# Kernel optimization log

Measured on AMD Instinct MI355X. Metric: run time of the kernel, lower is better.

Reference implementation:

```python
import jax, jax.numpy as jnp
import numpy as np

B, N, ND, ED, TD, H = 4, 256, 256, 64, 64, 8
D = ND // H
SCALE = np.float32(1.0 / np.sqrt(ND))
EPS = 1e-5


def leaky(x):
    return jnp.where(x >= 0, x, 0.05 * x)


def _ln(x, g, b):
    m = x.mean(axis=-1, keepdims=True)
    v = ((x - m) ** 2).mean(axis=-1, keepdims=True)
    return (x - m) * jax.lax.rsqrt(v + EPS) * g + b


def setup_inputs() -> dict:
    key = jax.random.key(0)
    ks = iter(jax.random.split(key, 64))

    def w(shape):
        return (jax.random.normal(next(ks), shape, jnp.float32) * 0.02).astype(jnp.float32)

    inp = {
        'nodes': jax.random.normal(next(ks), (B, N, ND), jnp.float32),
        'edges': jax.random.normal(next(ks), (B, N, N, ED), jnp.float32),
        'times': jax.random.normal(next(ks), (B, TD), jnp.float32),
        'Wq': w((ND + TD, ND)), 'bq': w((ND,)),
        'Wk': w((ND + TD, ND)), 'bk': w((ND,)),
        'Wv': w((ND + TD, ND)), 'bv': w((ND,)),
        'Wm': w((ED, ND)), 'bm': w((ND,)),
        'Wa': w((ED, ND)), 'ba': w((ND,)),
        'Wno': w((ND, ND)), 'bno': w((ND,)),
        'Weo': w((ND, ED)), 'beo': w((ED,)),
        'ln1n_g': jnp.ones((ND,), jnp.float32), 'ln1n_b': jnp.zeros((ND,), jnp.float32),
        'ln1e_g': jnp.ones((ED,), jnp.float32), 'ln1e_b': jnp.zeros((ED,), jnp.float32),
        'Wn1': w((ND, ND)), 'bn1': w((ND,)),
        'Wn2': w((ND, ND)), 'bn2': w((ND,)),
        'We1': w((ED, ED)), 'be1': w((ED,)),
        'We2': w((ED, ED)), 'be2': w((ED,)),
        'ln2n_g': jnp.ones((ND,), jnp.float32), 'ln2n_b': jnp.zeros((ND,), jnp.float32),
        'ln2e_g': jnp.ones((ED,), jnp.float32), 'ln2e_b': jnp.zeros((ED,), jnp.float32),
    }
    return inp


def reference(nodes, edges, times, Wq, bq, Wk, bk, Wv, bv, Wm, bm, Wa, ba,
              Wno, bno, Weo, beo, ln1n_g, ln1n_b, ln1e_g, ln1e_b,
              Wn1, bn1, Wn2, bn2, We1, be1, We2, be2,
              ln2n_g, ln2n_b, ln2e_g, ln2e_b):
    b, n, _ = nodes.shape
    # concat time embedding onto every node: [B, N, ND+TD]
    nt = jnp.concatenate([nodes, jnp.broadcast_to(times[:, None, :], (b, n, times.shape[-1]))], axis=-1)
    q = (nt @ Wq + bq).reshape(b, n, H, D)
    k = (nt @ Wk + bk).reshape(b, n, H, D)
    # all-pairs elementwise qk product: [B, N, N, H, D]
    attn = q[:, :, None, :, :] * k[:, None, :, :, :] * SCALE
    em = (edges @ Wm + bm).reshape(b, n, n, H, D)
    ea = (edges @ Wa + ba).reshape(b, n, n, H, D)
    new_edges = attn * em + attn + ea                    # [B,N,N,H,D]
    a = jax.nn.softmax(new_edges.sum(axis=4), axis=2)    # [B,N,N,H]
    v = (nt @ Wv + bv).reshape(b, n, H, D)
    wv = jnp.einsum('bijh,bjhd->bihd', a, v).reshape(b, n, ND)
    ne_flat = new_edges.reshape(b, n, n, ND)
    attn_nodes = wv @ Wno + bno                          # lin_nodes_out
    attn_edges = leaky(ne_flat) @ Weo + beo              # lin_edges_out
    attn_nodes = leaky(_ln(attn_nodes + nodes, ln1n_g, ln1n_b))
    attn_edges = _ln(attn_edges + edges, ln1e_g, ln1e_b)
    mn = leaky(attn_nodes @ Wn1 + bn1) @ Wn2 + bn2
    me = leaky(attn_edges @ We1 + be1) @ We2 + be2
    out_nodes = leaky(_ln(mn + attn_nodes, ln2n_g, ln2n_b))
    out_edges = _ln(me + attn_edges, ln2e_g, ln2e_b)
    return out_nodes, out_edges
```

## Files before the change

kernel.cpp:

```cpp
#include <hip/hip_runtime.h>
#include <hip/hip_bf16.h>

#define DEVFN __device__ __forceinline__

static constexpr float KSCALE = 0.0625f;
static constexpr float KEPS   = 1e-5f;

static constexpr int WS_Q   = 0;
static constexpr int WS_K   = 262144;
static constexpr int WS_V   = 524288;
static constexpr int WS_WNO = 1048576;
static constexpr int WS_WN1 = WS_WNO + 65536;
static constexpr int WS_WN2 = WS_WN1 + 65536;
static constexpr int WS_P   = WS_WN2 + 65536;
static constexpr int P_BQ=0, P_BK=256, P_BV=512, P_BM=768, P_BA=1024, P_BNO=1280,
  P_BEO=1536, P_LN1NG=1600, P_LN1NB=1856, P_LN1EG=2112, P_LN1EB=2176,
  P_BN1=2240, P_BN2=2496, P_BE1=2752, P_BE2=2816, P_LN2NG=2880, P_LN2NB=3136,
  P_LN2EG=3392, P_LN2EB=3456;
static constexpr int WS_BF  = WS_P + 3520;

typedef __attribute__((ext_vector_type(8))) short short8v;
typedef __attribute__((ext_vector_type(4))) float f32x4;
typedef __attribute__((ext_vector_type(4))) unsigned uint4v;
#define MFMA16(a, b, c) __builtin_amdgcn_mfma_f32_16x16x32_bf16((a), (b), (c), 0, 0, 0)

DEVFN float ldin(const void* p, int i, int bf) {
  if (bf) {
    unsigned short u = ((const unsigned short*)p)[i];
    return __uint_as_float(((unsigned)u) << 16);
  }
  return ((const float*)p)[i];
}
DEVFN unsigned short f2bf(float x) {
  unsigned b = __float_as_uint(x);
  b += 0x7FFFu + ((b >> 16) & 1u);
  return (unsigned short)(b >> 16);
}
DEVFN float bf2f(unsigned short u) { return __uint_as_float(((unsigned)u) << 16); }
DEVFN float lrelu(float x) { return x >= 0.f ? x : 0.05f * x; }
DEVFN int   dtflag(const void* l1ng) {
  return (((const unsigned*)l1ng)[0] != 0x3F800000u) ? 1 : 0;
}
DEVFN unsigned pack_bf2(float a, float b) {
  return ((unsigned)f2bf(b) << 16) | (unsigned)f2bf(a);
}
DEVFN short8v pack8(const float* p) {
  const float4 x0 = *(const float4*)p;
  const float4 x1 = *(const float4*)(p + 4);
  uint4v d;
  d[0] = pack_bf2(x0.x, x0.y); d[1] = pack_bf2(x0.z, x0.w);
  d[2] = pack_bf2(x1.x, x1.y); d[3] = pack_bf2(x1.z, x1.w);
  return __builtin_bit_cast(short8v, d);
}

__global__ __launch_bounds__(256) void k0_prep(float* __restrict__ wsf,
    const void* Wq, const void* bq, const void* Wk, const void* bk,
    const void* Wv, const void* bv, const void* Wm, const void* bm,
    const void* Wa, const void* ba, const void* Wno, const void* bno,
    const void* Weo, const void* beo, const void* l1ng, const void* l1nb,
    const void* l1eg, const void* l1eb, const void* Wn1, const void* bn1,
    const void* Wn2, const void* bn2, const void* We1, const void* be1,
    const void* We2, const void* be2, const void* l2ng, const void* l2nb,
    const void* l2eg, const void* l2eb)
{
  const int bf = dtflag(l1ng);
  const int g  = blockIdx.x * blockDim.x + threadIdx.x;
  const int gs = gridDim.x * blockDim.x;
  short* sb = (short*)(wsf + WS_BF);
#define CPY(src, off, n) for (int i = g; i < (n); i += gs) wsf[(off) + i] = ldin(src, i, bf)
  for (int i = g; i < 16384; i += gs) {
    int c = i >> 6, t = i & 63;
    sb[i]         = (short)f2bf(ldin(Wm, t * 256 + c, bf));
    sb[16384 + i] = (short)f2bf(ldin(Wa, t * 256 + c, bf));
  }
  for (int i = g; i < 16384; i += gs) {
    int u = i >> 8, c = i & 255;
    sb[32768 + i] = (short)f2bf(ldin(Weo, c * 64 + u, bf));
  }
  for (int i = g; i < 4096; i += gs) {
    int u = i >> 6, t = i & 63;
    sb[49152 + i] = (short)f2bf(ldin(We1, t * 64 + u, bf));
    sb[53248 + i] = (short)f2bf(ldin(We2, t * 64 + u, bf));
  }
  for (int i = g; i < 81920; i += gs) {
    int c = i / 320, t = i - c * 320;
    const int src = t * 256 + c;
    sb[57344 + i]  = (short)f2bf(ldin(Wq, src, bf));
    sb[139264 + i] = (short)f2bf(ldin(Wk, src, bf));
    sb[221184 + i] = (short)f2bf(ldin(Wv, src, bf));
  }
  CPY(Wno, WS_WNO, 65536);
  CPY(Wn1, WS_WN1, 65536);
  CPY(Wn2, WS_WN2, 65536);
  CPY(bq,  WS_P + P_BQ, 256);   CPY(bk,  WS_P + P_BK, 256);
  CPY(bv,  WS_P + P_BV, 256);   CPY(bm,  WS_P + P_BM, 256);
  CPY(ba,  WS_P + P_BA, 256);   CPY(bno, WS_P + P_BNO, 256);
  CPY(beo, WS_P + P_BEO, 64);
  CPY(l1ng, WS_P + P_LN1NG, 256); CPY(l1nb, WS_P + P_LN1NB, 256);
  CPY(l1eg, WS_P + P_LN1EG, 64);  CPY(l1eb, WS_P + P_LN1EB, 64);
  CPY(bn1, WS_P + P_BN1, 256);  CPY(bn2, WS_P + P_BN2, 256);
  CPY(be1, WS_P + P_BE1, 64);   CPY(be2, WS_P + P_BE2, 64);
  CPY(l2ng, WS_P + P_LN2NG, 256); CPY(l2nb, WS_P + P_LN2NB, 256);
  CPY(l2eg, WS_P + P_LN2EG, 64);  CPY(l2eb, WS_P + P_LN2EB, 64);
#undef CPY
}

__global__ __launch_bounds__(256) void k1_qkv(float* __restrict__ wsf,
    const void* nodes, const void* times, const void* l1ng)
{
  const int bf  = dtflag(l1ng);
  const int bid = blockIdx.x;
  const int b   = bid / 48;
  const int rem = bid - b * 48;
  const int mat = rem >> 4;
  const int n16 = rem & 15;
  const int tid = threadIdx.x;
  const int wv_ = tid >> 6;
  const int l   = tid & 63;
  const int l15 = l & 15, gq = l >> 4;

  const float* Pb = wsf + WS_P;
  const short* At = (const short*)(wsf + WS_BF) + 57344 + mat * 81920;
  const int n = (n16 << 4) + l15;

  short8v Bn[10];
  if (bf) {
    const unsigned short* np = (const unsigned short*)nodes + (size_t)(b * 256 + n) * 256;
#pragma unroll
    for (int kb = 0; kb < 8; ++kb)
      Bn[kb] = *(const short8v*)(np + (kb << 5) + (gq << 3));
    const unsigned short* tp = (const unsigned short*)times + b * 64;
#pragma unroll
    for (int kb = 8; kb < 10; ++kb)
      Bn[kb] = *(const short8v*)(tp + ((kb - 8) << 5) + (gq << 3));
  } else {
    const float* np = (const float*)nodes + (size_t)(b * 256 + n) * 256;
#pragma unroll
    for (int kb = 0; kb < 8; ++kb)
      Bn[kb] = pack8(np + (kb << 5) + (gq << 3));
    const float* tp = (const float*)times + b * 64;
#pragma unroll
    for (int kb = 8; kb < 10; ++kb)
      Bn[kb] = pack8(tp + ((kb - 8) << 5) + (gq << 3));
  }

  f32x4 acc[4];
#pragma unroll
  for (int cf = 0; cf < 4; ++cf) acc[cf] = f32x4{0.f, 0.f, 0.f, 0.f};
#pragma unroll
  for (int cf = 0; cf < 4; ++cf) {
    const int crow = ((wv_ << 6) + (cf << 4) + l15) * 320;
#pragma unroll
    for (int kb = 0; kb < 10; ++kb) {
      const short8v A = *(const short8v*)(At + crow + (kb << 5) + (gq << 3));
      acc[cf] = MFMA16(A, Bn[kb], acc[cf]);
    }
  }

  if (mat == 1) {
    float* dst = wsf + WS_K + b * 65536;
#pragma unroll
    for (int cf = 0; cf < 4; ++cf)
#pragma unroll
      for (int r = 0; r < 4; ++r) {
        const int c = (wv_ << 6) + (cf << 4) + (gq << 2) + r;
        dst[c * 256 + n] = acc[cf][r] + Pb[P_BK + c];
      }
  } else if (mat == 0) {
    float* dst = wsf + WS_Q + (size_t)(b * 256 + n) * 256;
#pragma unroll
    for (int cf = 0; cf < 4; ++cf)
#pragma unroll
      for (int r = 0; r < 4; ++r) {
        const int c = (wv_ << 6) + (cf << 4) + (gq << 2) + r;
        dst[c] = (acc[cf][r] + Pb[P_BQ + c]) * KSCALE;
      }
  } else {
    float* dst = wsf + WS_V + (size_t)(b * 256 + n) * 256;
#pragma unroll
    for (int cf = 0; cf < 4; ++cf)
#pragma unroll
      for (int r = 0; r < 4; ++r) {
        const int c = (wv_ << 6) + (cf << 4) + (gq << 2) + r;
        dst[c] = acc[cf][r] + Pb[P_BV + c];
      }
  }
}

DEVFN void bstats256(float v, float* red, float& mu, float& rs) {
  float s = v, q = v * v;
#pragma unroll
  for (int off = 32; off; off >>= 1) { s += __shfl_xor(s, off, 64); q += __shfl_xor(q, off, 64); }
  const int w = threadIdx.x >> 6;
  if ((threadIdx.x & 63) == 0) { red[w] = s; red[8 + w] = q; }
  __syncthreads();
  s = red[0] + red[1] + red[2] + red[3];
  q = red[8] + red[9] + red[10] + red[11];
  __syncthreads();
  mu = s * (1.f / 256.f);
  const float var = q * (1.f / 256.f) - mu * mu;
  rs = rsqrtf(var + KEPS);
}

__global__ __launch_bounds__(256, 2) void k2_edges(float* __restrict__ wsf,
    const void* edges, const void* nodes, void* __restrict__ out, const void* l1ng)
{
  const int bf  = dtflag(l1ng);
  const int bid = blockIdx.x;
  const int b   = bid >> 8;
  const int tid = threadIdx.x;
  const int wv_ = tid >> 6;
  const int l   = tid & 63;
  const int l15 = l & 15, gq = l >> 4;

  __shared__ float sl[8 * 256];
  __shared__ unsigned short ptile[4][4096];
  __shared__ float swv[256];
  __shared__ float red[16];

  const float* Pb = wsf + WS_P;
  const short* WmTb  = (const short*)(wsf + WS_BF);
  const short* WaTb  = WmTb + 16384;
  const short* WeoTb = WaTb + 16384;
  const short* We1Tb = WeoTb + 16384;
  const short* We2Tb = We1Tb + 4096;
  const float* kTb   = wsf + WS_K + b * 65536;

#pragma unroll
  for (int h = 0; h < 8; ++h) sl[(h << 8) + tid] = 0.f;

  short8v Ef[2][4];
#pragma unroll
  for (int jf = 0; jf < 4; ++jf) {
    const int jg = (wv_ << 6) + (jf << 4) + l15;
    const size_t ebase = (size_t)(bid * 256 + jg) * 64;
#pragma unroll
    for (int kb = 0; kb < 2; ++kb) {
      const int t0 = (kb << 5) + (gq << 3);
      if (bf) {
        Ef[kb][jf] = *(const short8v*)((const unsigned short*)edges + ebase + t0);
      } else {
        Ef[kb][jf] = pack8((const float*)edges + ebase + t0);
      }
    }
  }

  f32x4 Oacc[4][4];
#pragma unroll
  for (int uf = 0; uf < 4; ++uf)
#pragma unroll
    for (int jf = 0; jf < 4; ++jf) { Oacc[uf][jf] = f32x4{0.f, 0.f, 0.f, 0.f}; }

  char* myp = (char*)&ptile[wv_][0];
  const int swz = (l15 & 7) << 4;

#pragma unroll 1
  for (int chunk = 0; chunk < 4; ++chunk) {
#pragma unroll
    for (int ci = 0; ci < 4; ++ci) {
      const int cf = (chunk << 2) + ci;
      const int crow = ((cf << 4) + l15) << 6;
      const short8v Am0 = *(const short8v*)(WmTb + crow + (gq << 3));
      const short8v Am1 = *(const short8v*)(WmTb + crow + 32 + (gq << 3));
      const short8v Aa0 = *(const short8v*)(WaTb + crow + (gq << 3));
      const short8v Aa1 = *(const short8v*)(WaTb + crow + 32 + (gq << 3));
      const int ce = (cf << 4) + (gq << 2);
      const float4 q4  = *(const float4*)(wsf + WS_Q + (size_t)bid * 256 + ce);
      const float4 bm4 = *(const float4*)(Pb + P_BM + ce);
      const float4 ba4 = *(const float4*)(Pb + P_BA + ce);
      const int h = cf >> 1;
#pragma unroll
      for (int jf = 0; jf < 4; ++jf) {
        f32x4 em = f32x4{0.f, 0.f, 0.f, 0.f};
        f32x4 ea = f32x4{0.f, 0.f, 0.f, 0.f};
        em = MFMA16(Am0, Ef[0][jf], em);
        em = MFMA16(Am1, Ef[1][jf], em);
        ea = MFMA16(Aa0, Ef[0][jf], ea);
        ea = MFMA16(Aa1, Ef[1][jf], ea);
        const int jg = (wv_ << 6) + (jf << 4) + l15;
        const float kv0 = kTb[(ce + 0) * 256 + jg];
        const float kv1 = kTb[(ce + 1) * 256 + jg];
        const float kv2 = kTb[(ce + 2) * 256 + jg];
        const float kv3 = kTb[(ce + 3) * 256 + jg];
        const float ne0 = (q4.x * kv0) * (em[0] + bm4.x + 1.f) + (ea[0] + ba4.x);
        const float ne1 = (q4.y * kv1) * (em[1] + bm4.y + 1.f) + (ea[1] + ba4.y);
        const float ne2 = (q4.z * kv2) * (em[2] + bm4.z + 1.f) + (ea[2] + ba4.z);
        const float ne3 = (q4.w * kv3) * (em[3] + bm4.w + 1.f) + (ea[3] + ba4.w);
        float part = (ne0 + ne1) + (ne2 + ne3);
        part += __shfl_xor(part, 16, 64);
        part += __shfl_xor(part, 32, 64);
        if (gq == 0) sl[(h << 8) + jg] += part;
        const unsigned pd0 = pack_bf2(lrelu(ne0), lrelu(ne1));
        const unsigned pd1 = pack_bf2(lrelu(ne2), lrelu(ne3));
        const int jl = (jf << 4) + l15;
        const unsigned boff = (jl << 7) + ((unsigned)((ci << 5) + (gq << 3)) ^ swz);
        *(unsigned long long*)(myp + boff) = ((unsigned long long)pd1 << 32) | pd0;
      }
    }
    short8v Bp[2][4];
#pragma unroll
    for (int kb = 0; kb < 2; ++kb)
#pragma unroll
      for (int jf = 0; jf < 4; ++jf) {
        const int jl = (jf << 4) + l15;
        const unsigned boff = (jl << 7) + ((unsigned)((kb << 6) + (gq << 4)) ^ swz);
        Bp[kb][jf] = *(const short8v*)(myp + boff);
      }
#pragma unroll
    for (int uf = 0; uf < 4; ++uf) {
      const int urow = ((uf << 4) + l15) << 8;
      const int cb = chunk << 6;
      const short8v Aw0 = *(const short8v*)(WeoTb + urow + cb + (gq << 3));
      const short8v Aw1 = *(const short8v*)(WeoTb + urow + cb + 32 + (gq << 3));
#pragma unroll
      for (int jf = 0; jf < 4; ++jf) {
        Oacc[uf][jf] = MFMA16(Aw0, Bp[0][jf], Oacc[uf][jf]);
        Oacc[uf][jf] = MFMA16(Aw1, Bp[1][jf], Oacc[uf][jf]);
      }
    }
  }

#pragma unroll
  for (int uf = 0; uf < 4; ++uf)
#pragma unroll
    for (int jf = 0; jf < 4; ++jf) {
      const unsigned pd0 = pack_bf2(Oacc[uf][jf][0], Oacc[uf][jf][1]);
      const unsigned pd1 = pack_bf2(Oacc[uf][jf][2], Oacc[uf][jf][3]);
      const int jl = (jf << 4) + l15;
      const unsigned boff = (jl << 7) + ((unsigned)((uf << 5) + (gq << 3)) ^ swz);
      *(unsigned long long*)(myp + boff) = ((unsigned long long)pd1 << 32) | pd0;
    }

  __syncthreads();

  {
    const int h = tid >> 5, ll = tid & 31;
    float* row = sl + (h << 8);
    float pv[8];
    float m = -1e30f;
#pragma unroll
    for (int k2 = 0; k2 < 8; ++k2) { float x = row[ll + (k2 << 5)]; pv[k2] = x; m = fmaxf(m, x); }
#pragma unroll
    for (int off = 16; off; off >>= 1) m = fmaxf(m, __shfl_xor(m, off, 64));
    float sum = 0.f;
#pragma unroll
    for (int k2 = 0; k2 < 8; ++k2) { float p = __expf(pv[k2] - m); pv[k2] = p; sum += p; }
#pragma unroll
    for (int off = 16; off; off >>= 1) sum += __shfl_xor(sum, off, 64);
    const float inv = 1.f / sum;
#pragma unroll
    for (int k2 = 0; k2 < 8; ++k2) row[ll + (k2 << 5)] = pv[k2] * inv;
  }
  __syncthreads();

  {
    const int c = tid;
    const float* arow = sl + ((c >> 5) << 8);
    const float* vcol = wsf + WS_V + b * 65536 + c;
    float a0 = 0.f, a1 = 0.f, a2 = 0.f, a3 = 0.f;
    for (int jj = 0; jj < 256; jj += 4) {
      a0 = fmaf(arow[jj],     vcol[jj << 8],        a0);
      a1 = fmaf(arow[jj + 1], vcol[(jj + 1) << 8],  a1);
      a2 = fmaf(arow[jj + 2], vcol[(jj + 2) << 8],  a2);
      a3 = fmaf(arow[jj + 3], vcol[(jj + 3) << 8],  a3);
    }
    swv[c] = (a0 + a1) + (a2 + a3);
  }

  const int jl   = tid & 63;
  const int rswz = (jl & 7) << 4;
  float e[64];
  {
    float o[64];
#pragma unroll
    for (int s = 0; s < 8; ++s) {
      const short8v v = *(const short8v*)(myp + (jl << 7) + ((unsigned)(s << 4) ^ rswz));
#pragma unroll
      for (int e2 = 0; e2 < 8; ++e2) o[(s << 3) + e2] = bf2f((unsigned short)v[e2]);
    }
    const size_t ebase = (size_t)(bid * 256 + tid) * 64;
    if (bf) {
      const unsigned short* ep = (const unsigned short*)edges + ebase;
#pragma unroll
      for (int t = 0; t < 64; ++t) e[t] = bf2f(ep[t]);
    } else {
      const float4* ep = (const float4*)((const float*)edges + ebase);
#pragma unroll
      for (int t = 0; t < 16; ++t) {
        const float4 v4 = ep[t];
        e[4*t] = v4.x; e[4*t+1] = v4.y; e[4*t+2] = v4.z; e[4*t+3] = v4.w;
      }
    }
#pragma unroll
    for (int u = 0; u < 64; ++u) o[u] = o[u] + Pb[P_BEO + u] + e[u];
    float mu = 0.f;
#pragma unroll
    for (int u = 0; u < 64; ++u) mu += o[u];
    mu *= (1.f / 64.f);
    float s2 = 0.f;
#pragma unroll
    for (int u = 0; u < 64; ++u) { float d = o[u] - mu; s2 = fmaf(d, d, s2); }
    const float rs = rsqrtf(s2 * (1.f / 64.f) + KEPS);
#pragma unroll
    for (int u = 0; u < 64; ++u) e[u] = fmaf((o[u] - mu) * rs, Pb[P_LN1EG + u], Pb[P_LN1EB + u]);
#pragma unroll
    for (int u0 = 0; u0 < 64; u0 += 4) {
      const unsigned pd0 = pack_bf2(e[u0],     e[u0 + 1]);
      const unsigned pd1 = pack_bf2(e[u0 + 2], e[u0 + 3]);
      *(unsigned long long*)(myp + (jl << 7) + ((unsigned)(u0 << 1) ^ rswz)) =
        ((unsigned long long)pd1 << 32) | pd0;
    }
  }

  {
    short8v Bf[2][4];
#pragma unroll
    for (int kb = 0; kb < 2; ++kb)
#pragma unroll
      for (int jf = 0; jf < 4; ++jf) {
        const int jfl = (jf << 4) + l15;
        Bf[kb][jf] = *(const short8v*)(myp + (jfl << 7) + ((unsigned)((kb << 6) + (gq << 4)) ^ swz));
      }
    f32x4 Hc[4][4];
#pragma unroll
    for (int uf = 0; uf < 4; ++uf) {
      const int ur = ((uf << 4) + l15) << 6;
      const short8v A0 = *(const short8v*)(We1Tb + ur + (gq << 3));
      const short8v A1 = *(const short8v*)(We1Tb + ur + 32 + (gq << 3));
#pragma unroll
      for (int jf = 0; jf < 4; ++jf) {
        f32x4 hh = f32x4{0.f, 0.f, 0.f, 0.f};
        hh = MFMA16(A0, Bf[0][jf], hh);
        hh = MFMA16(A1, Bf[1][jf], hh);
        Hc[uf][jf] = hh;
      }
    }
#pragma unroll
    for (int uf = 0; uf < 4; ++uf) {
      const int u0 = (uf << 4) + (gq << 2);
      const float4 b14 = *(const float4*)(Pb + P_BE1 + u0);
#pragma unroll
      for (int jf = 0; jf < 4; ++jf) {
        const int jfl = (jf << 4) + l15;
        const unsigned pd0 = pack_bf2(lrelu(Hc[uf][jf][0] + b14.x), lrelu(Hc[uf][jf][1] + b14.y));
        const unsigned pd1 = pack_bf2(lrelu(Hc[uf][jf][2] + b14.z), lrelu(Hc[uf][jf][3] + b14.w));
        *(unsigned long long*)(myp + (jfl << 7) + ((unsigned)((uf << 5) + (gq << 3)) ^ swz)) =
          ((unsigned long long)pd1 << 32) | pd0;
      }
    }
#pragma unroll
    for (int kb = 0; kb < 2; ++kb)
#pragma unroll
      for (int jf = 0; jf < 4; ++jf) {
        const int jfl = (jf << 4) + l15;
        Bf[kb][jf] = *(const short8v*)(myp + (jfl << 7) + ((unsigned)((kb << 6) + (gq << 4)) ^ swz));
      }
#pragma unroll
    for (int uf = 0; uf < 4; ++uf) {
      const int ur = ((uf << 4) + l15) << 6;
      const short8v A0 = *(const short8v*)(We2Tb + ur + (gq << 3));
      const short8v A1 = *(const short8v*)(We2Tb + ur + 32 + (gq << 3));
      const int u0 = (uf << 4) + (gq << 2);
      const float4 b24 = *(const float4*)(Pb + P_BE2 + u0);
#pragma unroll
      for (int jf = 0; jf < 4; ++jf) {
        f32x4 mm = f32x4{0.f, 0.f, 0.f, 0.f};
        mm = MFMA16(A0, Bf[0][jf], mm);
        mm = MFMA16(A1, Bf[1][jf], mm);
        const int jfl = (jf << 4) + l15;
        const unsigned pd0 = pack_bf2(mm[0] + b24.x, mm[1] + b24.y);
        const unsigned pd1 = pack_bf2(mm[2] + b24.z, mm[3] + b24.w);
        *(unsigned long long*)(myp + (jfl << 7) + ((unsigned)((uf << 5) + (gq << 3)) ^ swz)) =
          ((unsigned long long)pd1 << 32) | pd0;
      }
    }
  }

  {
    float o[64];
#pragma unroll
    for (int s = 0; s < 8; ++s) {
      const short8v v = *(const short8v*)(myp + (jl << 7) + ((unsigned)(s << 4) ^ rswz));
#pragma unroll
      for (int e2 = 0; e2 < 8; ++e2) o[(s << 3) + e2] = bf2f((unsigned short)v[e2]);
    }
#pragma unroll
    for (int u = 0; u < 64; ++u) o[u] += e[u];
    float mu = 0.f;
#pragma unroll
    for (int u = 0; u < 64; ++u) mu += o[u];
    mu *= (1.f / 64.f);
    float s2 = 0.f;
#pragma unroll
    for (int u = 0; u < 64; ++u) { float d = o[u] - mu; s2 = fmaf(d, d, s2); }
    const float rs = rsqrtf(s2 * (1.f / 64.f) + KEPS);
    if (bf) {
      unsigned* op = (unsigned*)((unsigned short*)out + 262144 + (size_t)(bid * 256 + tid) * 64);
#pragma unroll
      for (int u = 0; u < 64; u += 2) {
        const float y0 = fmaf((o[u]     - mu) * rs, Pb[P_LN2EG + u],     Pb[P_LN2EB + u]);
        const float y1 = fmaf((o[u + 1] - mu) * rs, Pb[P_LN2EG + u + 1], Pb[P_LN2EB + u + 1]);
        op[u >> 1] = ((unsigned)f2bf(y1) << 16) | (unsigned)f2bf(y0);
      }
    } else {
      float4* op = (float4*)((float*)out + 262144 + (size_t)(bid * 256 + tid) * 64);
#pragma unroll
      for (int u = 0; u < 64; u += 4) {
        float4 y;
        y.x = fmaf((o[u]     - mu) * rs, Pb[P_LN2EG + u],     Pb[P_LN2EB + u]);
        y.y = fmaf((o[u + 1] - mu) * rs, Pb[P_LN2EG + u + 1], Pb[P_LN2EB + u + 1]);
        y.z = fmaf((o[u + 2] - mu) * rs, Pb[P_LN2EG + u + 2], Pb[P_LN2EB + u + 2]);
        y.w = fmaf((o[u + 3] - mu) * rs, Pb[P_LN2EG + u + 3], Pb[P_LN2EB + u + 3]);
        op[u >> 2] = y;
      }
    }
  }

  __syncthreads();
  {
    const int c = tid;
    float an = Pb[P_BNO + c];
    {
      const float* w = wsf + WS_WNO + c;
      float p0 = 0.f, p1 = 0.f, p2 = 0.f, p3 = 0.f;
      for (int t = 0; t < 256; t += 4) {
        p0 = fmaf(swv[t],     w[t << 8],       p0);
        p1 = fmaf(swv[t + 1], w[(t + 1) << 8], p1);
        p2 = fmaf(swv[t + 2], w[(t + 2) << 8], p2);
        p3 = fmaf(swv[t + 3], w[(t + 3) << 8], p3);
      }
      an += (p0 + p1) + (p2 + p3);
    }
    an += ldin(nodes, bid * 256 + c, bf);
    float mu, rs;
    bstats256(an, red, mu, rs);
    const float anf = lrelu(fmaf((an - mu) * rs, Pb[P_LN1NG + c], Pb[P_LN1NB + c]));
    __syncthreads();
    swv[c] = anf;
    __syncthreads();
    float h1 = Pb[P_BN1 + c];
    {
      const float* w = wsf + WS_WN1 + c;
      float p0 = 0.f, p1 = 0.f, p2 = 0.f, p3 = 0.f;
      for (int t = 0; t < 256; t += 4) {
        p0 = fmaf(swv[t],     w[t << 8],       p0);
        p1 = fmaf(swv[t + 1], w[(t + 1) << 8], p1);
        p2 = fmaf(swv[t + 2], w[(t + 2) << 8], p2);
        p3 = fmaf(swv[t + 3], w[(t + 3) << 8], p3);
      }
      h1 += (p0 + p1) + (p2 + p3);
    }
    h1 = lrelu(h1);
    __syncthreads();
    swv[c] = h1;
    __syncthreads();
    float mn = Pb[P_BN2 + c];
    {
      const float* w = wsf + WS_WN2 + c;
      float p0 = 0.f, p1 = 0.f, p2 = 0.f, p3 = 0.f;
      for (int t = 0; t < 256; t += 4) {
        p0 = fmaf(swv[t],     w[t << 8],       p0);
        p1 = fmaf(swv[t + 1], w[(t + 1) << 8], p1);
        p2 = fmaf(swv[t + 2], w[(t + 2) << 8], p2);
        p3 = fmaf(swv[t + 3], w[(t + 3) << 8], p3);
      }
      mn += (p0 + p1) + (p2 + p3);
    }
    const float x2 = mn + anf;
    bstats256(x2, red, mu, rs);
    const float y = lrelu(fmaf((x2 - mu) * rs, Pb[P_LN2NG + c], Pb[P_LN2NB + c]));
    if (bf) ((unsigned short*)out)[bid * 256 + c] = f2bf(y);
    else    ((float*)out)[bid * 256 + c] = y;
  }
}

extern "C" void kernel_launch(void* const* d_in, const int* in_sizes, int n_in,
                              void* d_out, int out_size, void* d_ws, size_t ws_size,
                              hipStream_t stream) {
  (void)in_sizes; (void)n_in; (void)out_size; (void)ws_size;
  float* wsf = (float*)d_ws;
  const void* nodes = d_in[0];
  const void* edges = d_in[1];
  const void* times = d_in[2];
  const void* l1ng  = d_in[17];

  k0_prep<<<128, 256, 0, stream>>>(wsf,
      d_in[3],  d_in[4],  d_in[5],  d_in[6],  d_in[7],  d_in[8],
      d_in[9],  d_in[10], d_in[11], d_in[12], d_in[13], d_in[14],
      d_in[15], d_in[16], d_in[17], d_in[18], d_in[19], d_in[20],
      d_in[21], d_in[22], d_in[23], d_in[24], d_in[25], d_in[26],
      d_in[27], d_in[28], d_in[29], d_in[30], d_in[31], d_in[32]);
  k1_qkv<<<192, 256, 0, stream>>>(wsf, nodes, times, l1ng);
  k2_edges<<<1024, 256, 0, stream>>>(wsf, edges, nodes, d_out, l1ng);
}
```

Measured before the change: 191.2 us.

## Double k2_edges block to 512 threads, splitting j rows and row-LN across lanes

The edge kernel now runs 512 threads per block, so each wave handles 32 edge rows instead of 64. Per-row LayerNorm work is split across two half-waves with a shuffle reduction, and the node-side matvecs and attention-weighted V sum are split in halves and combined through shared memory. The aim is to cut per-thread register pressure (the large float[64] arrays) and raise latency hiding. The cost is extra __syncthreads and partial-sum reductions, and launch_bounds(512,4) may force register spills.

```diff
diff --git a/kernel.cpp b/kernel.cpp
--- a/kernel.cpp
+++ b/kernel.cpp
@@ -187,22 +187,22 @@
   }
 }
 
-DEVFN void bstats256(float v, float* red, float& mu, float& rs) {
-  float s = v, q = v * v;
-#pragma unroll
-  for (int off = 32; off; off >>= 1) { s += __shfl_xor(s, off, 64); q += __shfl_xor(q, off, 64); }
-  const int w = threadIdx.x >> 6;
-  if ((threadIdx.x & 63) == 0) { red[w] = s; red[8 + w] = q; }
+DEVFN void bstats256_512(float v, float* red, int tid, float& mu, float& rs) {
+  if (tid < 256) {
+    float s = v, q = v * v;
+#pragma unroll
+    for (int off = 32; off; off >>= 1) { s += __shfl_xor(s, off, 64); q += __shfl_xor(q, off, 64); }
+    if ((tid & 63) == 0) { red[tid >> 6] = s; red[8 + (tid >> 6)] = q; }
+  }
   __syncthreads();
-  s = red[0] + red[1] + red[2] + red[3];
-  q = red[8] + red[9] + red[10] + red[11];
+  const float ss = (red[0] + red[1]) + (red[2] + red[3]);
+  const float qq = (red[8] + red[9]) + (red[10] + red[11]);
   __syncthreads();
-  mu = s * (1.f / 256.f);
-  const float var = q * (1.f / 256.f) - mu * mu;
-  rs = rsqrtf(var + KEPS);
-}
-
-__global__ __launch_bounds__(256, 2) void k2_edges(float* __restrict__ wsf,
+  mu = ss * (1.f / 256.f);
+  rs = rsqrtf(qq * (1.f / 256.f) - mu * mu + KEPS);
+}
+
+__global__ __launch_bounds__(512, 4) void k2_edges(float* __restrict__ wsf,
     const void* edges, const void* nodes, void* __restrict__ out, const void* l1ng)
 {
   const int bf  = dtflag(l1ng);
@@ -214,8 +214,9 @@
   const int l15 = l & 15, gq = l >> 4;
 
   __shared__ float sl[8 * 256];
-  __shared__ unsigned short ptile[4][4096];
+  __shared__ unsigned short ptile[8][2048];
   __shared__ float swv[256];
+  __shared__ float swv2[512];
   __shared__ float red[16];
 
   const float* Pb = wsf + WS_P;
@@ -227,12 +228,13 @@
   const float* kTb   = wsf + WS_K + b * 65536;
 
 #pragma unroll
-  for (int h = 0; h < 8; ++h) sl[(h << 8) + tid] = 0.f;
-
-  short8v Ef[2][4];
-#pragma unroll
-  for (int jf = 0; jf < 4; ++jf) {
-    const int jg = (wv_ << 6) + (jf << 4) + l15;
+  for (int i = 0; i < 4; ++i) sl[tid + (i << 9)] = 0.f;
+  __syncthreads();
+
+  short8v Ef[2][2];
+#pragma unroll
+  for (int jf = 0; jf < 2; ++jf) {
+    const int jg = (wv_ << 5) + (jf << 4) + l15;
     const size_t ebase = (size_t)(bid * 256 + jg) * 64;
 #pragma unroll
     for (int kb = 0; kb < 2; ++kb) {
@@ -245,11 +247,11 @@
     }
   }
 
-  f32x4 Oacc[4][4];
+  f32x4 Oacc[4][2];
 #pragma unroll
   for (int uf = 0; uf < 4; ++uf)
 #pragma unroll
-    for (int jf = 0; jf < 4; ++jf) { Oacc[uf][jf] = f32x4{0.f, 0.f, 0.f, 0.f}; }
+    for (int jf = 0; jf < 2; ++jf) { Oacc[uf][jf] = f32x4{0.f, 0.f, 0.f, 0.f}; }
 
   char* myp = (char*)&ptile[wv_][0];
   const int swz = (l15 & 7) << 4;
@@ -270,14 +272,14 @@
       const float4 ba4 = *(const float4*)(Pb + P_BA + ce);
       const int h = cf >> 1;
 #pragma unroll
-      for (int jf = 0; jf < 4; ++jf) {
+      for (int jf = 0; jf < 2; ++jf) {
         f32x4 em = f32x4{0.f, 0.f, 0.f, 0.f};
         f32x4 ea = f32x4{0.f, 0.f, 0.f, 0.f};
         em = MFMA16(Am0, Ef[0][jf], em);
         em = MFMA16(Am1, Ef[1][jf], em);
         ea = MFMA16(Aa0, Ef[0][jf], ea);
         ea = MFMA16(Aa1, Ef[1][jf], ea);
-        const int jg = (wv_ << 6) + (jf << 4) + l15;
+        const int jg = (wv_ << 5) + (jf << 4) + l15;
         const float kv0 = kTb[(ce + 0) * 256 + jg];
         const float kv1 = kTb[(ce + 1) * 256 + jg];
         const float kv2 = kTb[(ce + 2) * 256 + jg];
@@ -297,11 +299,11 @@
         *(unsigned long long*)(myp + boff) = ((unsigned long long)pd1 << 32) | pd0;
       }
     }
-    short8v Bp[2][4];
+    short8v Bp[2][2];
 #pragma unroll
     for (int kb = 0; kb < 2; ++kb)
 #pragma unroll
-      for (int jf = 0; jf < 4; ++jf) {
+      for (int jf = 0; jf < 2; ++jf) {
         const int jl = (jf << 4) + l15;
         const unsigned boff = (jl << 7) + ((unsigned)((kb << 6) + (gq << 4)) ^ swz);
         Bp[kb][jf] = *(const short8v*)(myp + boff);
@@ -313,7 +315,7 @@
       const short8v Aw0 = *(const short8v*)(WeoTb + urow + cb + (gq << 3));
       const short8v Aw1 = *(const short8v*)(WeoTb + urow + cb + 32 + (gq << 3));
 #pragma unroll
-      for (int jf = 0; jf < 4; ++jf) {
+      for (int jf = 0; jf < 2; ++jf) {
         Oacc[uf][jf] = MFMA16(Aw0, Bp[0][jf], Oacc[uf][jf]);
         Oacc[uf][jf] = MFMA16(Aw1, Bp[1][jf], Oacc[uf][jf]);
       }
@@ -323,7 +325,7 @@
 #pragma unroll
   for (int uf = 0; uf < 4; ++uf)
 #pragma unroll
-    for (int jf = 0; jf < 4; ++jf) {
+    for (int jf = 0; jf < 2; ++jf) {
       const unsigned pd0 = pack_bf2(Oacc[uf][jf][0], Oacc[uf][jf][1]);
       const unsigned pd1 = pack_bf2(Oacc[uf][jf][2], Oacc[uf][jf][3]);
       const int jl = (jf << 4) + l15;
@@ -334,101 +336,112 @@
   __syncthreads();
 
   {
-    const int h = tid >> 5, ll = tid & 31;
+    const int h = wv_;
     float* row = sl + (h << 8);
-    float pv[8];
+    float pv[4];
     float m = -1e30f;
 #pragma unroll
-    for (int k2 = 0; k2 < 8; ++k2) { float x = row[ll + (k2 << 5)]; pv[k2] = x; m = fmaxf(m, x); }
-#pragma unroll
-    for (int off = 16; off; off >>= 1) m = fmaxf(m, __shfl_xor(m, off, 64));
+    for (int k2 = 0; k2 < 4; ++k2) { float x = row[l + (k2 << 6)]; pv[k2] = x; m = fmaxf(m, x); }
+#pragma unroll
+    for (int off = 32; off; off >>= 1) m = fmaxf(m, __shfl_xor(m, off, 64));
     float sum = 0.f;
 #pragma unroll
-    for (int k2 = 0; k2 < 8; ++k2) { float p = __expf(pv[k2] - m); pv[k2] = p; sum += p; }
-#pragma unroll
-    for (int off = 16; off; off >>= 1) sum += __shfl_xor(sum, off, 64);
+    for (int k2 = 0; k2 < 4; ++k2) { float p = __expf(pv[k2] - m); pv[k2] = p; sum += p; }
+#pragma unroll
+    for (int off = 32; off; off >>= 1) sum += __shfl_xor(sum, off, 64);
     const float inv = 1.f / sum;
 #pragma unroll
-    for (int k2 = 0; k2 < 8; ++k2) row[ll + (k2 << 5)] = pv[k2] * inv;
+    for (int k2 = 0; k2 < 4; ++k2) row[l + (k2 << 6)] = pv[k2] * inv;
   }
   __syncthreads();
 
   {
-    const int c = tid;
+    const int c = tid & 255, jh = tid >> 8;
     const float* arow = sl + ((c >> 5) << 8);
     const float* vcol = wsf + WS_V + b * 65536 + c;
+    const int j0 = jh << 7;
     float a0 = 0.f, a1 = 0.f, a2 = 0.f, a3 = 0.f;
-    for (int jj = 0; jj < 256; jj += 4) {
+    for (int jj = j0; jj < j0 + 128; jj += 4) {
       a0 = fmaf(arow[jj],     vcol[jj << 8],        a0);
       a1 = fmaf(arow[jj + 1], vcol[(jj + 1) << 8],  a1);
       a2 = fmaf(arow[jj + 2], vcol[(jj + 2) << 8],  a2);
       a3 = fmaf(arow[jj + 3], vcol[(jj + 3) << 8],  a3);
     }
-    swv[c] = (a0 + a1) + (a2 + a3);
-  }
-
-  const int jl   = tid & 63;
-  const int rswz = (jl & 7) << 4;
-  float e[64];
+    swv2[tid] = (a0 + a1) + (a2 + a3);
+  }
+  __syncthreads();
+  if (tid < 256) swv[tid] = swv2[tid] + swv2[tid + 256];
+
+  const int r    = l & 31;
+  const int hf   = l >> 5;
+  const int jrow = (wv_ << 5) + r;
+  const int u0   = hf << 5;
+  const int rswz = (r & 7) << 4;
+  float ae[32];
   {
-    float o[64];
-#pragma unroll
-    for (int s = 0; s < 8; ++s) {
-      const short8v v = *(const short8v*)(myp + (jl << 7) + ((unsigned)(s << 4) ^ rswz));
-#pragma unroll
-      for (int e2 = 0; e2 < 8; ++e2) o[(s << 3) + e2] = bf2f((unsigned short)v[e2]);
-    }
-    const size_t ebase = (size_t)(bid * 256 + tid) * 64;
+    float xr[32];
+#pragma unroll
+    for (int s4 = 0; s4 < 4; ++s4) {
+      const int s = (hf << 2) + s4;
+      const short8v v = *(const short8v*)(myp + (r << 7) + ((unsigned)(s << 4) ^ rswz));
+#pragma unroll
+      for (int e2 = 0; e2 < 8; ++e2) xr[(s4 << 3) + e2] = bf2f((unsigned short)v[e2]);
+    }
+    const size_t ebase = (size_t)(bid * 256 + jrow) * 64 + u0;
     if (bf) {
       const unsigned short* ep = (const unsigned short*)edges + ebase;
 #pragma unroll
-      for (int t = 0; t < 64; ++t) e[t] = bf2f(ep[t]);
+      for (int k = 0; k < 32; ++k) xr[k] += Pb[P_BEO + u0 + k] + bf2f(ep[k]);
     } else {
-      const float4* ep = (const float4*)((const float*)edges + ebase);
-#pragma unroll
-      for (int t = 0; t < 16; ++t) {
-        const float4 v4 = ep[t];
-        e[4*t] = v4.x; e[4*t+1] = v4.y; e[4*t+2] = v4.z; e[4*t+3] = v4.w;
-      }
-    }
-#pragma unroll
-    for (int u = 0; u < 64; ++u) o[u] = o[u] + Pb[P_BEO + u] + e[u];
-    float mu = 0.f;
-#pragma unroll
-    for (int u = 0; u < 64; ++u) mu += o[u];
-    mu *= (1.f / 64.f);
-    float s2 = 0.f;
-#pragma unroll
-    for (int u = 0; u < 64; ++u) { float d = o[u] - mu; s2 = fmaf(d, d, s2); }
-    const float rs = rsqrtf(s2 * (1.f / 64.f) + KEPS);
-#pragma unroll
-    for (int u = 0; u < 64; ++u) e[u] = fmaf((o[u] - mu) * rs, Pb[P_LN1EG + u], Pb[P_LN1EB + u]);
-#pragma unroll
-    for (int u0 = 0; u0 < 64; u0 += 4) {
-      const unsigned pd0 = pack_bf2(e[u0],     e[u0 + 1]);
-      const unsigned pd1 = pack_bf2(e[u0 + 2], e[u0 + 3]);
-      *(unsigned long long*)(myp + (jl << 7) + ((unsigned)(u0 << 1) ^ rswz)) =
+      const float* ep = (const float*)edges + ebase;
+#pragma unroll
+      for (int k = 0; k < 32; k += 4) {
+        const float4 v4 = *(const float4*)(ep + k);
+        xr[k]     += Pb[P_BEO + u0 + k]     + v4.x;
+        xr[k + 1] += Pb[P_BEO + u0 + k + 1] + v4.y;
+        xr[k + 2] += Pb[P_BEO + u0 + k + 2] + v4.z;
+        xr[k + 3] += Pb[P_BEO + u0 + k + 3] + v4.w;
+      }
+    }
+    float s = 0.f;
+#pragma unroll
+    for (int k = 0; k < 32; ++k) s += xr[k];
+    s += __shfl_xor(s, 32, 64);
+    const float mu = s * (1.f / 64.f);
+    float q = 0.f;
+#pragma unroll
+    for (int k = 0; k < 32; ++k) { const float d = xr[k] - mu; q = fmaf(d, d, q); }
+    q += __shfl_xor(q, 32, 64);
+    const float rstd = rsqrtf(q * (1.f / 64.f) + KEPS);
+#pragma unroll
+    for (int k = 0; k < 32; ++k)
+      ae[k] = fmaf((xr[k] - mu) * rstd, Pb[P_LN1EG + u0 + k], Pb[P_LN1EB + u0 + k]);
+#pragma unroll
+    for (int k = 0; k < 32; k += 4) {
+      const unsigned pd0 = pack_bf2(ae[k],     ae[k + 1]);
+      const unsigned pd1 = pack_bf2(ae[k + 2], ae[k + 3]);
+      *(unsigned long long*)(myp + (r << 7) + ((unsigned)((u0 + k) << 1) ^ rswz)) =
         ((unsigned long long)pd1 << 32) | pd0;
     }
   }
 
   {
-    short8v Bf[2][4];
+    short8v Bf[2][2];
 #pragma unroll
     for (int kb = 0; kb < 2; ++kb)
 #pragma unroll
-      for (int jf = 0; jf < 4; ++jf) {
+      for (int jf = 0; jf < 2; ++jf) {
         const int jfl = (jf << 4) + l15;
         Bf[kb][jf] = *(const short8v*)(myp + (jfl << 7) + ((unsigned)((kb << 6) + (gq << 4)) ^ swz));
       }
-    f32x4 Hc[4][4];
+    f32x4 Hc[4][2];
 #pragma unroll
     for (int uf = 0; uf < 4; ++uf) {
       const int ur = ((uf << 4) + l15) << 6;
       const short8v A0 = *(const short8v*)(We1Tb + ur + (gq << 3));
       const short8v A1 = *(const short8v*)(We1Tb + ur + 32 + (gq << 3));
 #pragma unroll
-      for (int jf = 0; jf < 4; ++jf) {
+      for (int jf = 0; jf < 2; ++jf) {
         f32x4 hh = f32x4{0.f, 0.f, 0.f, 0.f};
         hh = MFMA16(A0, Bf[0][jf], hh);
         hh = MFMA16(A1, Bf[1][jf], hh);
@@ -437,10 +450,10 @@
     }
 #pragma unroll
     for (int uf = 0; uf < 4; ++uf) {
-      const int u0 = (uf << 4) + (gq << 2);
-      const float4 b14 = *(const float4*)(Pb + P_BE1 + u0);
-#pragma unroll
-      for (int jf = 0; jf < 4; ++jf) {
+      const int uu = (uf << 4) + (gq << 2);
+      const float4 b14 = *(const float4*)(Pb + P_BE1 + uu);
+#pragma unroll
+      for (int jf = 0; jf < 2; ++jf) {
         const int jfl = (jf << 4) + l15;
         const unsigned pd0 = pack_bf2(lrelu(Hc[uf][jf][0] + b14.x), lrelu(Hc[uf][jf][1] + b14.y));
         const unsigned pd1 = pack_bf2(lrelu(Hc[uf][jf][2] + b14.z), lrelu(Hc[uf][jf][3] + b14.w));
@@ -451,7 +464,7 @@
 #pragma unroll
     for (int kb = 0; kb < 2; ++kb)
 #pragma unroll
-      for (int jf = 0; jf < 4; ++jf) {
+      for (int jf = 0; jf < 2; ++jf) {
         const int jfl = (jf << 4) + l15;
         Bf[kb][jf] = *(const short8v*)(myp + (jfl << 7) + ((unsigned)((kb << 6) + (gq << 4)) ^ swz));
       }
@@ -460,10 +473,10 @@
       const int ur = ((uf << 4) + l15) << 6;
       const short8v A0 = *(const short8v*)(We2Tb + ur + (gq << 3));
       const short8v A1 = *(const short8v*)(We2Tb + ur + 32 + (gq << 3));
-      const int u0 = (uf << 4) + (gq << 2);
-      const float4 b24 = *(const float4*)(Pb + P_BE2 + u0);
-#pragma unroll
-      for (int jf = 0; jf < 4; ++jf) {
+      const int uu = (uf << 4) + (gq << 2);
+      const float4 b24 = *(const float4*)(Pb + P_BE2 + uu);
+#pragma unroll
+      for (int jf = 0; jf < 2; ++jf) {
         f32x4 mm = f32x4{0.f, 0.f, 0.f, 0.f};
         mm = MFMA16(A0, Bf[0][jf], mm);
         mm = MFMA16(A1, Bf[1][jf], mm);
@@ -477,100 +490,109 @@
   }
 
   {
-    float o[64];
-#pragma unroll
-    for (int s = 0; s < 8; ++s) {
-      const short8v v = *(const short8v*)(myp + (jl << 7) + ((unsigned)(s << 4) ^ rswz));
-#pragma unroll
-      for (int e2 = 0; e2 < 8; ++e2) o[(s << 3) + e2] = bf2f((unsigned short)v[e2]);
-    }
-#pragma unroll
-    for (int u = 0; u < 64; ++u) o[u] += e[u];
-    float mu = 0.f;
-#pragma unroll
-    for (int u = 0; u < 64; ++u) mu += o[u];
-    mu *= (1.f / 64.f);
-    float s2 = 0.f;
-#pragma unroll
-    for (int u = 0; u < 64; ++u) { float d = o[u] - mu; s2 = fmaf(d, d, s2); }
-    const float rs = rsqrtf(s2 * (1.f / 64.f) + KEPS);
+    float xr[32];
+#pragma unroll
+    for (int s4 = 0; s4 < 4; ++s4) {
+      const int s = (hf << 2) + s4;
+      const short8v v = *(const short8v*)(myp + (r << 7) + ((unsigned)(s << 4) ^ rswz));
+#pragma unroll
+      for (int e2 = 0; e2 < 8; ++e2) xr[(s4 << 3) + e2] = bf2f((unsigned short)v[e2]);
+    }
+#pragma unroll
+    for (int k = 0; k < 32; ++k) xr[k] += ae[k];
+    float s = 0.f;
+#pragma unroll
+    for (int k = 0; k < 32; ++k) s += xr[k];
+    s += __shfl_xor(s, 32, 64);
+    const float mu = s * (1.f / 64.f);
+    float q = 0.f;
+#pragma unroll
+    for (int k = 0; k < 32; ++k) { const float d = xr[k] - mu; q = fmaf(d, d, q); }
+    q += __shfl_xor(q, 32, 64);
+    const float rstd = rsqrtf(q * (1.f / 64.f) + KEPS);
     if (bf) {
-      unsigned* op = (unsigned*)((unsigned short*)out + 262144 + (size_t)(bid * 256 + tid) * 64);
-#pragma unroll
-      for (int u = 0; u < 64; u += 2) {
-        const float y0 = fmaf((o[u]     - mu) * rs, Pb[P_LN2EG + u],     Pb[P_LN2EB + u]);
-        const float y1 = fmaf((o[u + 1] - mu) * rs, Pb[P_LN2EG + u + 1], Pb[P_LN2EB + u + 1]);
-        op[u >> 1] = ((unsigned)f2bf(y1) << 16) | (unsigned)f2bf(y0);
+      unsigned long long* op = (unsigned long long*)
+        ((unsigned short*)out + 262144 + (size_t)(bid * 256 + jrow) * 64 + u0);
+#pragma unroll
+      for (int k = 0; k < 32; k += 4) {
+        const float y0 = fmaf((xr[k]     - mu) * rstd, Pb[P_LN2EG + u0 + k],     Pb[P_LN2EB + u0 + k]);
+        const float y1 = fmaf((xr[k + 1] - mu) * rstd, Pb[P_LN2EG + u0 + k + 1], Pb[P_LN2EB + u0 + k + 1]);
+        const float y2 = fmaf((xr[k + 2] - mu) * rstd, Pb[P_LN2EG + u0 + k + 2], Pb[P_LN2EB + u0 + k + 2]);
+        const float y3 = fmaf((xr[k + 3] - mu) * rstd, Pb[P_LN2EG + u0 + k + 3], Pb[P_LN2EB + u0 + k + 3]);
+        op[k >> 2] = ((unsigned long long)pack_bf2(y2, y3) << 32) | pack_bf2(y0, y1);
       }
     } else {
-      float4* op = (float4*)((float*)out + 262144 + (size_t)(bid * 256 + tid) * 64);
-#pragma unroll
-      for (int u = 0; u < 64; u += 4) {
+      float4* op = (float4*)((float*)out + 262144 + (size_t)(bid * 256 + jrow) * 64 + u0);
+#pragma unroll
+      for (int k = 0; k < 32; k += 4) {
         float4 y;
-        y.x = fmaf((o[u]     - mu) * rs, Pb[P_LN2EG + u],     Pb[P_LN2EB + u]);
-        y.y = fmaf((o[u + 1] - mu) * rs, Pb[P_LN2EG + u + 1], Pb[P_LN2EB + u + 1]);
-        y.z = fmaf((o[u + 2] - mu) * rs, Pb[P_LN2EG + u + 2], Pb[P_LN2EB + u + 2]);
-        y.w = fmaf((o[u + 3] - mu) * rs, Pb[P_LN2EG + u + 3], Pb[P_LN2EB + u + 3]);
-        op[u >> 2] = y;
+        y.x = fmaf((xr[k]     - mu) * rstd, Pb[P_LN2EG + u0 + k],     Pb[P_LN2EB + u0 + k]);
+        y.y = fmaf((xr[k + 1] - mu) * rstd, Pb[P_LN2EG + u0 + k + 1], Pb[P_LN2EB + u0 + k + 1]);
+        y.z = fmaf((xr[k + 2] - mu) * rstd, Pb[P_LN2EG + u0 + k + 2], Pb[P_LN2EB + u0 + k + 2]);
+        y.w = fmaf((xr[k + 3] - mu) * rstd, Pb[P_LN2EG + u0 + k + 3], Pb[P_LN2EB + u0 + k + 3]);
+        op[k >> 2] = y;
       }
     }
   }
 
   __syncthreads();
   {
-    const int c = tid;
-    float an = Pb[P_BNO + c];
+    const int c = tid & 255, th = tid >> 8;
+    const int t0 = th << 7;
     {
       const float* w = wsf + WS_WNO + c;
       float p0 = 0.f, p1 = 0.f, p2 = 0.f, p3 = 0.f;
-      for (int t = 0; t < 256; t += 4) {
+      for (int t = t0; t < t0 + 128; t += 4) {
         p0 = fmaf(swv[t],     w[t << 8],       p0);
         p1 = fmaf(swv[t + 1], w[(t + 1) << 8], p1);
         p2 = fmaf(swv[t + 2], w[(t + 2) << 8], p2);
         p3 = fmaf(swv[t + 3], w[(t + 3) << 8], p3);
       }
-      an += (p0 + p1) + (p2 + p3);
-    }
-    an += ldin(nodes, bid * 256 + c, bf);
+      swv2[tid] = (p0 + p1) + (p2 + p3);
+    }
+    __syncthreads();
+    float an = Pb[P_BNO + c] + swv2[c] + swv2[256 + c] + ldin(nodes, bid * 256 + c, bf);
     float mu, rs;
-    bstats256(an, red, mu, rs);
+    bstats256_512(an, red, tid, mu, rs);
     const float anf = lrelu(fmaf((an - mu) * rs, Pb[P_LN1NG + c], Pb[P_LN1NB + c]));
+    if (tid < 256) swv[c] = anf;
     __syncthreads();
-    swv[c] = anf;
-    __syncthreads();
-    float h1 = Pb[P_BN1 + c];
     {
       const float* w = wsf + WS_WN1 + c;
       float p0 = 0.f, p1 = 0.f, p2 = 0.f, p3 = 0.f;
-      for (int t = 0; t < 256; t += 4) {
+      for (int t = t0; t < t0 + 128; t += 4) {
         p0 = fmaf(swv[t],     w[t << 8],       p0);
         p1 = fmaf(swv[t + 1], w[(t + 1) << 8], p1);
         p2 = fmaf(swv[t + 2], w[(t + 2) << 8], p2);
         p3 = fmaf(swv[t + 3], w[(t + 3) << 8], p3);
       }
-      h1 += (p0 + p1) + (p2 + p3);
-    }
-    h1 = lrelu(h1);
+      swv2[tid] = (p0 + p1) + (p2 + p3);
+    }
     __syncthreads();
-    swv[c] = h1;
+    const float h1v = lrelu(Pb[P_BN1 + c] + swv2[c] + swv2[256 + c]);
     __syncthreads();
-    float mn = Pb[P_BN2 + c];
+    if (tid < 256) swv[c] = h1v;
+    __syncthreads();
     {
       const float* w = wsf + WS_WN2 + c;
       float p0 = 0.f, p1 = 0.f, p2 = 0.f, p3 = 0.f;
-      for (int t = 0; t < 256; t += 4) {
+      for (int t = t0; t < t0 + 128; t += 4) {
         p0 = fmaf(swv[t],     w[t << 8],       p0);
         p1 = fmaf(swv[t + 1], w[(t + 1) << 8], p1);
         p2 = fmaf(swv[t + 2], w[(t + 2) << 8], p2);
         p3 = fmaf(swv[t + 3], w[(t + 3) << 8], p3);
       }
-      mn += (p0 + p1) + (p2 + p3);
-    }
+      swv2[tid] = (p0 + p1) + (p2 + p3);
+    }
+    __syncthreads();
+    const float mn = Pb[P_BN2 + c] + swv2[c] + swv2[256 + c];
     const float x2 = mn + anf;
-    bstats256(x2, red, mu, rs);
-    const float y = lrelu(fmaf((x2 - mu) * rs, Pb[P_LN2NG + c], Pb[P_LN2NB + c]));
-    if (bf) ((unsigned short*)out)[bid * 256 + c] = f2bf(y);
-    else    ((float*)out)[bid * 256 + c] = y;
+    bstats256_512(x2, red, tid, mu, rs);
+    if (tid < 256) {
+      const float y = lrelu(fmaf((x2 - mu) * rs, Pb[P_LN2NG + c], Pb[P_LN2NB + c]));
+      if (bf) ((unsigned short*)out)[bid * 256 + c] = f2bf(y);
+      else    ((float*)out)[bid * 256 + c] = y;
+    }
   }
 }
 
@@ -591,5 +613,5 @@
       d_in[21], d_in[22], d_in[23], d_in[24], d_in[25], d_in[26],
       d_in[27], d_in[28], d_in[29], d_in[30], d_in[31], d_in[32]);
   k1_qkv<<<192, 256, 0, stream>>>(wsf, nodes, times, l1ng);
-  k2_edges<<<1024, 256, 0, stream>>>(wsf, edges, nodes, d_out, l1ng);
-}
+  k2_edges<<<1024, 512, 0, stream>>>(wsf, edges, nodes, d_out, l1ng);
+}
```

New measurement: 323.5 us. 1.69x slower.
